# Optimization experiments

Measured on AMD Instinct MI355X. Metric: run time of the kernel, lower is better.

The kernel has to match this reference:

```python
import jax, jax.numpy as jnp
import numpy as np

B, S, D, F, E = 8, 4096, 512, 2048, 8


def setup_inputs() -> dict:
    key = jax.random.key(0)
    ks = jax.random.split(key, 10)
    std = 0.02
    return {
        "x": jax.random.normal(ks[0], (B, S, D), dtype=jnp.float32),
        "gate_w": jax.random.normal(ks[1], (D, E), dtype=jnp.float32) * std,
        "gate_b": jnp.zeros((E,), dtype=jnp.float32),
        "w1": jax.random.normal(ks[2], (E, D, F), dtype=jnp.float32) * std,
        "b1": jnp.zeros((E, F), dtype=jnp.float32),
        "w2": jax.random.normal(ks[3], (E, D, F), dtype=jnp.float32) * std,
        "b2": jnp.zeros((E, F), dtype=jnp.float32),
        "w3": jax.random.normal(ks[4], (E, F, D), dtype=jnp.float32) * std,
        "b3": jnp.zeros((E, D), dtype=jnp.float32),
    }


def reference(x, gate_w, gate_b, w1, b1, w2, b2, w3, b3):
    b, s, d = x.shape
    xt = x.reshape(-1, d)                      # [N, D]
    logits = xt @ gate_w + gate_b              # [N, E]
    top = jnp.argmax(logits, axis=-1)          # [N] top-1 expert per token
    soft = jax.nn.softmax(logits, axis=-1)     # [N, E]
    num_experts = gate_w.shape[1]

    out = jnp.zeros_like(xt)
    # Loop over the small fixed expert set; weight is zero where a token
    # is not routed to expert i, reproducing masked dispatch+combine math.
    for i in range(num_experts):
        h = jax.nn.gelu(xt @ w1[i] + b1[i], approximate=False) * (xt @ w2[i] + b2[i])
        y = h @ w3[i] + b3[i]                  # [N, D]
        w = jnp.where(top == i, soft[:, i], 0.0)[:, None]
        out = out + w * y

    aux_loss = jnp.asarray(0.0, dtype=x.dtype)  # eval mode: no aux loss
    return out.reshape(b, s, d), aux_loss
```

## Files before the change

kernel.cpp:

```cpp
#include <hip/hip_runtime.h>
#include <hip/hip_bf16.h>

typedef unsigned short u16;
typedef __bf16 bf16x8 __attribute__((ext_vector_type(8)));
typedef float f32x4 __attribute__((ext_vector_type(4)));

#define N_TOK 32768
#define DD 512
#define FF 2048
#define EE 8

#define CTL_CNT 0
#define CTL_CUR 8
#define CTL_OFF 16
#define CTL_NT 25
#define CTL_TE 32
#define CTL_TI 304

__device__ inline u16 f2bu(float f) {
  unsigned u = __builtin_bit_cast(unsigned, f);
  unsigned r = (u + 0x7fffu + ((u >> 16) & 1u)) >> 16;
  return (u16)r;
}

__device__ inline f32x4 mfma16(bf16x8 a, bf16x8 b, f32x4 c) {
  return __builtin_amdgcn_mfma_f32_16x16x32_bf16(a, b, c, 0, 0, 0);
}

__device__ inline void gload_lds16(const void* g, void* l) {
  __builtin_amdgcn_global_load_lds(
      (const __attribute__((address_space(1))) void*)g,
      (__attribute__((address_space(3))) void*)l, 16, 0, 0);
}


__global__ void gate_k(const float* __restrict__ x, const float* __restrict__ gw,
                       const float* __restrict__ gb, int* __restrict__ eid,
                       float* __restrict__ wgt, u16* __restrict__ Xb) {
  __shared__ float gws[DD * 9];
  for (int i = threadIdx.x; i < DD * EE; i += 256)
    gws[(i >> 3) * 9 + (i & 7)] = gw[i];
  __syncthreads();
  const int tok = (int)((blockIdx.x * 256 + threadIdx.x) >> 6);
  const int lane = threadIdx.x & 63;
  const float* xr = x + (size_t)tok * DD;

  const float4 v0 = *(const float4*)(xr + lane * 8);
  const float4 v1 = *(const float4*)(xr + lane * 8 + 4);
  union { u16 u[8]; uint4 v; } o;
  o.u[0] = f2bu(v0.x); o.u[1] = f2bu(v0.y); o.u[2] = f2bu(v0.z); o.u[3] = f2bu(v0.w);
  o.u[4] = f2bu(v1.x); o.u[5] = f2bu(v1.y); o.u[6] = f2bu(v1.z); o.u[7] = f2bu(v1.w);
  *reinterpret_cast<uint4*>(Xb + (size_t)tok * DD + lane * 8) = o.v;

  float a[EE];
#pragma unroll
  for (int e = 0; e < EE; ++e) a[e] = 0.f;
#pragma unroll
  for (int i = 0; i < 8; ++i) {
    const int d = lane + i * 64;
    const float xv = xr[d];
#pragma unroll
    for (int e = 0; e < EE; ++e) a[e] += xv * gws[d * 9 + e];
  }
#pragma unroll
  for (int e = 0; e < EE; ++e) {
#pragma unroll
    for (int off = 32; off > 0; off >>= 1) a[e] += __shfl_xor(a[e], off);
  }
  if (lane == 0) {
    float m = -1e30f; int bi = 0;
#pragma unroll
    for (int e = 0; e < EE; ++e) {
      const float l2 = a[e] + gb[e];
      a[e] = l2;
      if (l2 > m) { m = l2; bi = e; }
    }
    float s = 0.f;
#pragma unroll
    for (int e = 0; e < EE; ++e) s += expf(a[e] - m);
    eid[tok] = bi;
    wgt[tok] = 1.f / s;
  }
}

__global__ void count_k(const int* __restrict__ eid, int* __restrict__ ctl) {
  __shared__ int h[EE];
  if (threadIdx.x < EE) h[threadIdx.x] = 0;
  __syncthreads();
  atomicAdd(&h[eid[blockIdx.x * 256 + threadIdx.x]], 1);
  __syncthreads();
  if (threadIdx.x < EE) atomicAdd(&ctl[CTL_CNT + threadIdx.x], h[threadIdx.x]);
}

__global__ void scan_k(int* __restrict__ ctl, float* __restrict__ aux) {
  __shared__ int tstart[EE + 1];
  if (threadIdx.x == 0) {
    int o = 0, nt = 0;
    for (int e = 0; e < EE; ++e) {
      ctl[CTL_OFF + e] = o;
      ctl[CTL_CUR + e] = o;
      tstart[e] = nt;
      const int c = ctl[CTL_CNT + e];
      nt += (c + 127) >> 7;
      o += c;
    }
    tstart[EE] = nt;
    ctl[CTL_OFF + 8] = o;
    ctl[CTL_NT] = nt;
    *aux = 0.f;
  }
  __syncthreads();
  const int nt = tstart[EE];
  for (int i = threadIdx.x; i < nt; i += 256) {
    int e = 0;
    while (tstart[e + 1] <= i) ++e;
    ctl[CTL_TE + i] = e;
    ctl[CTL_TI + i] = i - tstart[e];
  }
}

__global__ void pos_k(const int* __restrict__ eid, const float* __restrict__ wgt,
                      int* __restrict__ ctl, int* __restrict__ sorted,
                      float* __restrict__ wgt_s) {
  __shared__ int h[EE], base[EE];
  const int t = blockIdx.x * 256 + threadIdx.x;
  if (threadIdx.x < EE) h[threadIdx.x] = 0;
  __syncthreads();
  const int e = eid[t];
  const int r = atomicAdd(&h[e], 1);
  __syncthreads();
  if (threadIdx.x < EE)
    base[threadIdx.x] = atomicAdd(&ctl[CTL_CUR + threadIdx.x], h[threadIdx.x]);
  __syncthreads();
  const int p = base[e] + r;
  sorted[p] = t;
  wgt_s[p] = wgt[t];
}

__global__ void transp_k(const float* __restrict__ in, u16* __restrict__ out,
                         int R, int C) {
  __shared__ u16 tile[64][66];
  const int e = blockIdx.z;
  const int c0 = blockIdx.x * 64, r0 = blockIdx.y * 64;
  const float* ip = in + (size_t)e * R * C;
  u16* op = out + (size_t)e * R * C;
  const int tx = threadIdx.x & 63, ty = threadIdx.x >> 6;
#pragma unroll
  for (int k = 0; k < 16; ++k) {
    const int r = ty * 16 + k;
    tile[r][tx] = f2bu(ip[(size_t)(r0 + r) * C + c0 + tx]);
  }
  __syncthreads();
#pragma unroll
  for (int k = 0; k < 16; ++k) {
    const int c = ty * 16 + k;
    op[(size_t)(c0 + c) * R + r0 + tx] = tile[tx][c];
  }
}

__global__ __launch_bounds__(256, 2) void gemm1_k(
    const u16* __restrict__ Xb, const u16* __restrict__ W1t,
    const u16* __restrict__ W2t, const float* __restrict__ b1,
    const float* __restrict__ b2, u16* __restrict__ Hbuf,
    const int* __restrict__ sorted, const int* __restrict__ ctl) {
  const int bx = blockIdx.x;
  if (bx >= ctl[CTL_NT]) return;
  const int e = ctl[CTL_TE + bx];
  const int ti = ctl[CTL_TI + bx];
  const int cnt = ctl[CTL_CNT + e];
  const int row0 = ctl[CTL_OFF + e] + ti * 128;
  const int rows = min(128, cnt - ti * 128);
  const int n0 = blockIdx.y * 128;

  __shared__ u16 As[2][4096];
  __shared__ u16 B1s[2][4096];
  __shared__ u16 B2s[2][4096];

  const u16* B1b = W1t + ((size_t)e * FF + n0) * DD;
  const u16* B2b = W2t + ((size_t)e * FF + n0) * DD;

  const int t = threadIdx.x;
  const u16 *aSrc[2], *b1Src[2], *b2Src[2];
  int dofs[2];
#pragma unroll
  for (int s = 0; s < 2; ++s) {
    const int Gp = s * 256 + t;
    const int r = ((Gp >> 3) << 1) | (((Gp >> 2) ^ (Gp >> 4)) & 1);
    const int g = (Gp & 3) ^ (r & 3);
    dofs[s] = Gp * 8;
    const int idx = min(row0 + r, N_TOK - 1);
    aSrc[s]  = Xb + (size_t)sorted[idx] * DD + g * 8;
    b1Src[s] = B1b + (size_t)r * DD + g * 8;
    b2Src[s] = B2b + (size_t)r * DD + g * 8;
  }
  auto stage_all = [&](int buf, int kc) {
#pragma unroll
    for (int s = 0; s < 2; ++s) gload_lds16(aSrc[s] + kc, &As[buf][dofs[s]]);
#pragma unroll
    for (int s = 0; s < 2; ++s) gload_lds16(b1Src[s] + kc, &B1s[buf][dofs[s]]);
#pragma unroll
    for (int s = 0; s < 2; ++s) gload_lds16(b2Src[s] + kc, &B2s[buf][dofs[s]]);
  };

  const f32x4 z = {0.f, 0.f, 0.f, 0.f};
  f32x4 acc1[4][4], acc2[4][4];
#pragma unroll
  for (int i = 0; i < 4; ++i)
#pragma unroll
    for (int j = 0; j < 4; ++j) { acc1[i][j] = z; acc2[i][j] = z; }

  stage_all(0, 0);
  asm volatile("s_waitcnt vmcnt(0)" ::: "memory");
  __syncthreads();

  const int lane = threadIdx.x & 63;
  const int w = t >> 6;
  const int wr = w >> 1, wc = w & 1;
  const int l15 = lane & 15, g8 = (lane >> 4) * 8, xv = (lane & 7) << 3;
  int offA[4], offB[4];
#pragma unroll
  for (int i = 0; i < 4; ++i) {
    offA[i] = (((wr * 64 + i * 16 + l15) * 32 + g8) ^ xv);
    offB[i] = (((wc * 64 + i * 16 + l15) * 32 + g8) ^ xv);
  }

  int cur = 0;
  for (int kt = 0; kt < 16; ++kt) {
    if (kt < 15) stage_all(cur ^ 1, (kt + 1) * 32);
    bf16x8 af[4], bf1[4], bf2[4];
#pragma unroll
    for (int mi = 0; mi < 4; ++mi)
      af[mi] = *(const bf16x8*)&As[cur][offA[mi]];
#pragma unroll
    for (int ni = 0; ni < 4; ++ni) {
      bf1[ni] = *(const bf16x8*)&B1s[cur][offB[ni]];
      bf2[ni] = *(const bf16x8*)&B2s[cur][offB[ni]];
    }
#pragma unroll
    for (int mi = 0; mi < 4; ++mi)
#pragma unroll
      for (int ni = 0; ni < 4; ++ni) {
        acc1[mi][ni] = mfma16(af[mi], bf1[ni], acc1[mi][ni]);
        acc2[mi][ni] = mfma16(af[mi], bf2[ni], acc2[mi][ni]);
      }
    asm volatile("s_waitcnt vmcnt(0)" ::: "memory");
    __syncthreads();
    cur ^= 1;
  }

#pragma unroll
  for (int mi = 0; mi < 4; ++mi) {
#pragma unroll
    for (int ni = 0; ni < 4; ++ni) {
      const int c = wc * 64 + ni * 16 + (lane & 15);
      const float bb1 = b1[(size_t)e * FF + n0 + c];
      const float bb2 = b2[(size_t)e * FF + n0 + c];
#pragma unroll
      for (int j = 0; j < 4; ++j) {
        const int r = wr * 64 + mi * 16 + (lane >> 4) * 4 + j;
        if (r < rows) {
          const float v1 = acc1[mi][ni][j] + bb1;
          const float v2 = acc2[mi][ni][j] + bb2;
          const float h = 0.5f * v1 * (1.f + erff(v1 * 0.70710678118f)) * v2;
          Hbuf[(size_t)(row0 + r) * FF + n0 + c] = f2bu(h);
        }
      }
    }
  }
}

__global__ __launch_bounds__(256, 2) void gemm2_k(
    const u16* __restrict__ Hbuf, const u16* __restrict__ W3t,
    const float* __restrict__ b3, const int* __restrict__ sorted,
    const float* __restrict__ wgt_s, float* __restrict__ out,
    const int* __restrict__ ctl) {
  const int bx = blockIdx.x;
  if (bx >= ctl[CTL_NT]) return;
  const int e = ctl[CTL_TE + bx];
  const int ti = ctl[CTL_TI + bx];
  const int cnt = ctl[CTL_CNT + e];
  const int row0 = ctl[CTL_OFF + e] + ti * 128;
  const int rows = min(128, cnt - ti * 128);
  const int n0 = blockIdx.y * 128;

  __shared__ u16 As[2][4096];
  __shared__ u16 Bs[2][4096];
  const u16* Ab = Hbuf + (size_t)row0 * FF;
  const u16* Bb = W3t + ((size_t)e * DD + n0) * FF;

  const int t = threadIdx.x;
  const u16 *aSrc[2], *bSrc[2];
  int dofs[2];
#pragma unroll
  for (int s = 0; s < 2; ++s) {
    const int Gp = s * 256 + t;
    const int r = ((Gp >> 3) << 1) | (((Gp >> 2) ^ (Gp >> 4)) & 1);
    const int g = (Gp & 3) ^ (r & 3);
    dofs[s] = Gp * 8;
    aSrc[s] = Ab + (size_t)r * FF + g * 8;
    bSrc[s] = Bb + (size_t)r * FF + g * 8;
  }
  auto stage_all = [&](int buf, int kc) {
#pragma unroll
    for (int s = 0; s < 2; ++s) gload_lds16(aSrc[s] + kc, &As[buf][dofs[s]]);
#pragma unroll
    for (int s = 0; s < 2; ++s) gload_lds16(bSrc[s] + kc, &Bs[buf][dofs[s]]);
  };

  const f32x4 z = {0.f, 0.f, 0.f, 0.f};
  f32x4 acc[4][4];
#pragma unroll
  for (int i = 0; i < 4; ++i)
#pragma unroll
    for (int j = 0; j < 4; ++j) acc[i][j] = z;

  stage_all(0, 0);
  asm volatile("s_waitcnt vmcnt(0)" ::: "memory");
  __syncthreads();

  const int lane = threadIdx.x & 63;
  const int w = t >> 6;
  const int wr = w >> 1, wc = w & 1;
  const int l15 = lane & 15, g8 = (lane >> 4) * 8, xv = (lane & 7) << 3;
  int offA[4], offB[4];
#pragma unroll
  for (int i = 0; i < 4; ++i) {
    offA[i] = (((wr * 64 + i * 16 + l15) * 32 + g8) ^ xv);
    offB[i] = (((wc * 64 + i * 16 + l15) * 32 + g8) ^ xv);
  }

  int cur = 0;
  for (int kt = 0; kt < 64; ++kt) {
    if (kt < 63) stage_all(cur ^ 1, (kt + 1) * 32);
    bf16x8 af[4], bf[4];
#pragma unroll
    for (int mi = 0; mi < 4; ++mi)
      af[mi] = *(const bf16x8*)&As[cur][offA[mi]];
#pragma unroll
    for (int ni = 0; ni < 4; ++ni)
      bf[ni] = *(const bf16x8*)&Bs[cur][offB[ni]];
#pragma unroll
    for (int mi = 0; mi < 4; ++mi)
#pragma unroll
      for (int ni = 0; ni < 4; ++ni)
        acc[mi][ni] = mfma16(af[mi], bf[ni], acc[mi][ni]);
    asm volatile("s_waitcnt vmcnt(0)" ::: "memory");
    __syncthreads();
    cur ^= 1;
  }

#pragma unroll
  for (int mi = 0; mi < 4; ++mi) {
#pragma unroll
    for (int ni = 0; ni < 4; ++ni) {
      const int c = wc * 64 + ni * 16 + (lane & 15);
      const float bb3 = b3[(size_t)e * DD + n0 + c];
#pragma unroll
      for (int j = 0; j < 4; ++j) {
        const int r = wr * 64 + mi * 16 + (lane >> 4) * 4 + j;
        if (r < rows) {
          const int p = row0 + r;
          const int tok = sorted[p];
          out[(size_t)tok * DD + n0 + c] = wgt_s[p] * (acc[mi][ni][j] + bb3);
        }
      }
    }
  }
}

extern "C" void kernel_launch(void* const* d_in, const int* in_sizes, int n_in,
                              void* d_out, int out_size, void* d_ws, size_t ws_size,
                              hipStream_t stream) {
  const float* x  = (const float*)d_in[0];
  const float* gw = (const float*)d_in[1];
  const float* gb = (const float*)d_in[2];
  const float* w1 = (const float*)d_in[3];
  const float* b1 = (const float*)d_in[4];
  const float* w2 = (const float*)d_in[5];
  const float* b2 = (const float*)d_in[6];
  const float* w3 = (const float*)d_in[7];
  const float* b3 = (const float*)d_in[8];
  float* out = (float*)d_out;

  char* base = (char*)d_ws;
  size_t off = 0;
  auto take = [&](size_t bytes) {
    char* r = base + off;
    off += (bytes + 255) & ~(size_t)255;
    return r;
  };
  int*   ctl    = (int*)take(4096);
  int*   eid    = (int*)take((size_t)N_TOK * 4);
  float* wgt    = (float*)take((size_t)N_TOK * 4);
  int*   sorted = (int*)take((size_t)(N_TOK + 128) * 4);
  float* wgt_s  = (float*)take((size_t)(N_TOK + 128) * 4);
  u16*   Xb     = (u16*)take((size_t)N_TOK * DD * 2);
  u16*   W1t    = (u16*)take((size_t)EE * FF * DD * 2);
  u16*   W2t    = (u16*)take((size_t)EE * FF * DD * 2);
  u16*   W3t    = (u16*)take((size_t)EE * DD * FF * 2);
  u16*   Hbuf   = (u16*)take((size_t)(N_TOK + 128) * FF * 2);

  hipMemsetAsync(ctl, 0, 64, stream);

  gate_k<<<8192, 256, 0, stream>>>(x, gw, gb, eid, wgt, Xb);
  count_k<<<128, 256, 0, stream>>>(eid, ctl);
  scan_k<<<1, 256, 0, stream>>>(ctl, out + (size_t)N_TOK * DD);
  pos_k<<<128, 256, 0, stream>>>(eid, wgt, ctl, sorted, wgt_s);

  transp_k<<<dim3(32, 8, EE), 256, 0, stream>>>(w1, W1t, 512, 2048);
  transp_k<<<dim3(32, 8, EE), 256, 0, stream>>>(w2, W2t, 512, 2048);
  transp_k<<<dim3(8, 32, EE), 256, 0, stream>>>(w3, W3t, 2048, 512);

  gemm1_k<<<dim3(264, 16), 256, 0, stream>>>(Xb, W1t, W2t, b1, b2, Hbuf, sorted, ctl);
  gemm2_k<<<dim3(264, 4), 256, 0, stream>>>(Hbuf, W3t, b3, sorted, wgt_s, out, ctl);
}
```

Before: 620.0 us.

## Triple-buffer LDS staging with partial vmcnt waits and MFMA priority boost

```diff
diff --git a/kernel.cpp b/kernel.cpp
--- a/kernel.cpp
+++ b/kernel.cpp
@@ -172,9 +172,9 @@
   const int rows = min(128, cnt - ti * 128);
   const int n0 = blockIdx.y * 128;
 
-  __shared__ u16 As[2][4096];
-  __shared__ u16 B1s[2][4096];
-  __shared__ u16 B2s[2][4096];
+  __shared__ u16 As[3][4096];
+  __shared__ u16 B1s[3][4096];
+  __shared__ u16 B2s[3][4096];
 
   const u16* B1b = W1t + ((size_t)e * FF + n0) * DD;
   const u16* B2b = W2t + ((size_t)e * FF + n0) * DD;
@@ -209,10 +209,6 @@
 #pragma unroll
     for (int j = 0; j < 4; ++j) { acc1[i][j] = z; acc2[i][j] = z; }
 
-  stage_all(0, 0);
-  asm volatile("s_waitcnt vmcnt(0)" ::: "memory");
-  __syncthreads();
-
   const int lane = threadIdx.x & 63;
   const int w = t >> 6;
   const int wr = w >> 1, wc = w & 1;
@@ -224,18 +220,20 @@
     offB[i] = (((wc * 64 + i * 16 + l15) * 32 + g8) ^ xv);
   }
 
-  int cur = 0;
-  for (int kt = 0; kt < 16; ++kt) {
-    if (kt < 15) stage_all(cur ^ 1, (kt + 1) * 32);
+  stage_all(0, 0);
+  stage_all(1, 32);
+
+  auto compute = [&](int buf) {
     bf16x8 af[4], bf1[4], bf2[4];
 #pragma unroll
     for (int mi = 0; mi < 4; ++mi)
-      af[mi] = *(const bf16x8*)&As[cur][offA[mi]];
+      af[mi] = *(const bf16x8*)&As[buf][offA[mi]];
 #pragma unroll
     for (int ni = 0; ni < 4; ++ni) {
-      bf1[ni] = *(const bf16x8*)&B1s[cur][offB[ni]];
-      bf2[ni] = *(const bf16x8*)&B2s[cur][offB[ni]];
+      bf1[ni] = *(const bf16x8*)&B1s[buf][offB[ni]];
+      bf2[ni] = *(const bf16x8*)&B2s[buf][offB[ni]];
     }
+    __builtin_amdgcn_s_setprio(1);
 #pragma unroll
     for (int mi = 0; mi < 4; ++mi)
 #pragma unroll
@@ -243,10 +241,18 @@
         acc1[mi][ni] = mfma16(af[mi], bf1[ni], acc1[mi][ni]);
         acc2[mi][ni] = mfma16(af[mi], bf2[ni], acc2[mi][ni]);
       }
-    asm volatile("s_waitcnt vmcnt(0)" ::: "memory");
+    __builtin_amdgcn_s_setprio(0);
+  };
+
+  for (int kt = 0; kt < 15; ++kt) {
+    asm volatile("s_waitcnt vmcnt(6)" ::: "memory");
     __syncthreads();
-    cur ^= 1;
-  }
+    if (kt < 14) stage_all((kt + 2) % 3, (kt + 2) * 32);
+    compute(kt % 3);
+  }
+  asm volatile("s_waitcnt vmcnt(0)" ::: "memory");
+  __syncthreads();
+  compute(15 % 3);
 
 #pragma unroll
   for (int mi = 0; mi < 4; ++mi) {
@@ -283,8 +289,8 @@
   const int rows = min(128, cnt - ti * 128);
   const int n0 = blockIdx.y * 128;
 
-  __shared__ u16 As[2][4096];
-  __shared__ u16 Bs[2][4096];
+  __shared__ u16 As[3][4096];
+  __shared__ u16 Bs[3][4096];
   const u16* Ab = Hbuf + (size_t)row0 * FF;
   const u16* Bb = W3t + ((size_t)e * DD + n0) * FF;
 
@@ -314,10 +320,6 @@
 #pragma unroll
     for (int j = 0; j < 4; ++j) acc[i][j] = z;
 
-  stage_all(0, 0);
-  asm volatile("s_waitcnt vmcnt(0)" ::: "memory");
-  __syncthreads();
-
   const int lane = threadIdx.x & 63;
   const int w = t >> 6;
   const int wr = w >> 1, wc = w & 1;
@@ -329,25 +331,35 @@
     offB[i] = (((wc * 64 + i * 16 + l15) * 32 + g8) ^ xv);
   }
 
-  int cur = 0;
-  for (int kt = 0; kt < 64; ++kt) {
-    if (kt < 63) stage_all(cur ^ 1, (kt + 1) * 32);
+  stage_all(0, 0);
+  stage_all(1, 32);
+
+  auto compute = [&](int buf) {
     bf16x8 af[4], bf[4];
 #pragma unroll
     for (int mi = 0; mi < 4; ++mi)
-      af[mi] = *(const bf16x8*)&As[cur][offA[mi]];
+      af[mi] = *(const bf16x8*)&As[buf][offA[mi]];
 #pragma unroll
     for (int ni = 0; ni < 4; ++ni)
-      bf[ni] = *(const bf16x8*)&Bs[cur][offB[ni]];
+      bf[ni] = *(const bf16x8*)&Bs[buf][offB[ni]];
+    __builtin_amdgcn_s_setprio(1);
 #pragma unroll
     for (int mi = 0; mi < 4; ++mi)
 #pragma unroll
       for (int ni = 0; ni < 4; ++ni)
         acc[mi][ni] = mfma16(af[mi], bf[ni], acc[mi][ni]);
-    asm volatile("s_waitcnt vmcnt(0)" ::: "memory");
+    __builtin_amdgcn_s_setprio(0);
+  };
+
+  for (int kt = 0; kt < 63; ++kt) {
+    asm volatile("s_waitcnt vmcnt(4)" ::: "memory");
     __syncthreads();
-    cur ^= 1;
-  }
+    if (kt < 62) stage_all((kt + 2) % 3, (kt + 2) * 32);
+    compute(kt % 3);
+  }
+  asm volatile("s_waitcnt vmcnt(0)" ::: "memory");
+  __syncthreads();
+  compute(63 % 3);
 
 #pragma unroll
   for (int mi = 0; mi < 4; ++mi) {
```

New measurement: 608.7 us. About the same (-1.8%).
